# Performance work log

Measured on AMD Instinct MI355X. Metric: run time of the kernel, lower is better.

## Reference

```python
import jax, jax.numpy as jnp
import numpy as np

DIM = 768
HEADS = 12
HEAD_DIM = DIM // HEADS
HIDDEN = 4 * DIM
SCALE = HEAD_DIM ** -0.5
LN_EPS = 1e-5


def layer_norm(x, g, b):
    mu = jnp.mean(x, axis=-1, keepdims=True)
    var = jnp.var(x, axis=-1, keepdims=True)
    return (x - mu) * jax.lax.rsqrt(var + LN_EPS) * g + b


def setup_inputs() -> dict:
    key = jax.random.key(0)
    ks = jax.random.split(key, 10)
    B, N = 2, 2048
    s = 0.02
    return {
        "x": jax.random.normal(ks[0], (B, N, DIM), jnp.float32),
        "elevation": jax.random.uniform(ks[1], (B, N), jnp.float32),
        "qkv_w": jax.random.normal(ks[2], (DIM, 3 * DIM), jnp.float32) * s,
        "qkv_b": jnp.zeros((3 * DIM,), jnp.float32),
        "proj_w": jax.random.normal(ks[3], (DIM, DIM), jnp.float32) * s,
        "proj_b": jnp.zeros((DIM,), jnp.float32),
        "ln1_g": jnp.ones((DIM,), jnp.float32),
        "ln1_b": jnp.zeros((DIM,), jnp.float32),
        "ln2_g": jnp.ones((DIM,), jnp.float32),
        "ln2_b": jnp.zeros((DIM,), jnp.float32),
        "fc1_w": jax.random.normal(ks[4], (DIM, HIDDEN), jnp.float32) * s,
        "fc1_b": jnp.zeros((HIDDEN,), jnp.float32),
        "fc2_w": jax.random.normal(ks[5], (HIDDEN, DIM), jnp.float32) * s,
        "fc2_b": jnp.zeros((DIM,), jnp.float32),
        "barrier": jnp.asarray(3.0, jnp.float32),
    }


def reference(x, elevation, qkv_w, qkv_b, proj_w, proj_b, ln1_g, ln1_b,
              ln2_g, ln2_b, fc1_w, fc1_b, fc2_w, fc2_b, barrier):
    B, N, C = x.shape
    h = layer_norm(x, ln1_g, ln1_b)
    qkv = (h @ qkv_w + qkv_b).reshape(B, N, 3, HEADS, HEAD_DIM)
    q, k, v = jnp.moveaxis(qkv, 2, 0)  # each [B, N, H, D]
    # scores: [B, H, N, N]
    scores = jnp.einsum('bnhd,bmhd->bhnm', q, k) * SCALE
    w = jax.nn.softmax(scores, axis=-1)
    # pairwise elevation mask [B, N, N]: sigmoid(-s * (elev_j - elev_i))
    diff = elevation[:, None, :] - elevation[:, :, None]
    mask = jnp.clip(jax.nn.sigmoid(-barrier * diff), 1e-6, 1.0)
    w = w * mask[:, None, :, :]
    w = w / (jnp.sum(w, axis=-1, keepdims=True) + 1e-8)
    attn_out = jnp.einsum('bhnm,bmhd->bnhd', w, v).reshape(B, N, C)
    x = x + attn_out @ proj_w + proj_b
    h2 = layer_norm(x, ln2_g, ln2_b)
    mlp = jax.nn.gelu(h2 @ fc1_w + fc1_b, approximate=False) @ fc2_w + fc2_b
    return x + mlp
```

## Files before the change

kernel.cpp:

```cpp
#include <hip/hip_runtime.h>
#include <math.h>

#define DIM 768
#define HEADS 12
#define SEQ 2048
#define ROWS 4096
#define LN_EPS 1e-5f

typedef __attribute__((ext_vector_type(8))) short short8;
typedef __attribute__((ext_vector_type(4))) float floatx4;
typedef __attribute__((ext_vector_type(16))) float floatx16;
typedef unsigned short ushort_t;

__device__ __forceinline__ ushort_t f2bf(float x) {
    unsigned u = __float_as_uint(x);
    u += 0x7fff + ((u >> 16) & 1);
    return (ushort_t)(u >> 16);
}

__device__ __forceinline__ void gload_lds16(const void* g, void* l) {
    __builtin_amdgcn_global_load_lds((const __attribute__((address_space(1))) void*)g,
                                     (__attribute__((address_space(3))) void*)l, 16, 0, 0);
}

__launch_bounds__(256)
__global__ void wconv_all(const float* __restrict__ w0, const float* __restrict__ w1,
                          const float* __restrict__ w2, const float* __restrict__ w3,
                          ushort_t* __restrict__ t0, ushort_t* __restrict__ t1,
                          ushort_t* __restrict__ t2, ushort_t* __restrict__ t3) {
    __shared__ __align__(16) ushort_t s[64][72];
    int bid = blockIdx.x;
    const float* W; ushort_t* WT; int K, N, nx, id;
    if (bid < 432)       { W = w0; WT = t0; K = 768;  N = 2304; nx = 36; id = bid; }
    else if (bid < 576)  { W = w1; WT = t1; K = 768;  N = 768;  nx = 12; id = bid - 432; }
    else if (bid < 1152) { W = w2; WT = t2; K = 768;  N = 3072; nx = 48; id = bid - 576; }
    else                 { W = w3; WT = t3; K = 3072; N = 768;  nx = 12; id = bid - 1152; }
    int tx = id % nx, ty = id / nx;
    int k0 = ty * 64, n0 = tx * 64;
    int t = threadIdx.x;
    int rr0 = t >> 4, c4 = (t & 15) * 4;
    for (int rr = rr0; rr < 64; rr += 16) {
        float4 w = *(const float4*)(W + (size_t)(k0 + rr) * N + n0 + c4);
        s[c4 + 0][rr] = f2bf(w.x); s[c4 + 1][rr] = f2bf(w.y);
        s[c4 + 2][rr] = f2bf(w.z); s[c4 + 3][rr] = f2bf(w.w);
    }
    __syncthreads();
    int nl = t >> 2, kq = (t & 3) * 16;
    uint4 a = *(const uint4*)&s[nl][kq];
    uint4 b = *(const uint4*)&s[nl][kq + 8];
    *(uint4*)(WT + (size_t)(n0 + nl) * K + k0 + kq) = a;
    *(uint4*)(WT + (size_t)(n0 + nl) * K + k0 + kq + 8) = b;
}

__launch_bounds__(256)
__global__ void gelev_kernel(const float* __restrict__ elev, const float* __restrict__ barrier_p,
                             float* __restrict__ G, float* __restrict__ C2) {
    int i = blockIdx.x * 256 + threadIdx.x;
    float be = barrier_p[0] * elev[i];
    G[i]  = __expf(be);
    C2[i] = be;
}

__launch_bounds__(256)
__global__ void ln_kernel(const float* __restrict__ x, const float* __restrict__ g,
                          const float* __restrict__ b, ushort_t* __restrict__ out) {
    int row = blockIdx.x;
    const float* xr = x + (size_t)row * DIM;
    int t = threadIdx.x;
    float v0 = xr[t], v1 = xr[t + 256], v2 = xr[t + 512];
    float s  = v0 + v1 + v2;
    float ss = v0 * v0 + v1 * v1 + v2 * v2;
    #pragma unroll
    for (int o = 32; o >= 1; o >>= 1) { s += __shfl_xor(s, o); ss += __shfl_xor(ss, o); }
    __shared__ float rs[4], rss[4];
    int wid = t >> 6, lane = t & 63;
    if (lane == 0) { rs[wid] = s; rss[wid] = ss; }
    __syncthreads();
    if (t == 0) {
        float S = 0.f, SS = 0.f;
        for (int i = 0; i < 4; i++) { S += rs[i]; SS += rss[i]; }
        rs[0] = S; rss[0] = SS;
    }
    __syncthreads();
    float mean = rs[0] * (1.0f / DIM);
    float var  = rss[0] * (1.0f / DIM) - mean * mean;
    float rstd = rsqrtf(var + LN_EPS);
    ushort_t* orow = out + (size_t)row * DIM;
    orow[t]       = f2bf((v0 - mean) * rstd * g[t]       + b[t]);
    orow[t + 256] = f2bf((v1 - mean) * rstd * g[t + 256] + b[t + 256]);
    orow[t + 512] = f2bf((v2 - mean) * rstd * g[t + 512] + b[t + 512]);
}

template<int EPI>
__launch_bounds__(256)
__global__ void gemm32(const ushort_t* __restrict__ A, const ushort_t* __restrict__ WT,
                       const float* __restrict__ bias, ushort_t* __restrict__ outB,
                       ushort_t* __restrict__ qb, ushort_t* __restrict__ kb,
                       ushort_t* __restrict__ vb, int N, int K) {
    __shared__ __align__(16) ushort_t sA[128 * 32];
    __shared__ __align__(16) ushort_t sB[128 * 32];
    int t = threadIdx.x;
    int row0 = blockIdx.y * 128, col0 = blockIdx.x * 128;
    int wid = t >> 6, lane = t & 63, l31 = lane & 31, hb = lane >> 5;
    int wm = wid >> 1, wn = wid & 1;

    floatx16 acc[2][2];
    #pragma unroll
    for (int i = 0; i < 2; i++)
        #pragma unroll
        for (int j = 0; j < 2; j++)
            #pragma unroll
            for (int e = 0; e < 16; e++) acc[i][j][e] = 0.f;

    for (int k0 = 0; k0 < K; k0 += 32) {
        #pragma unroll
        for (int i = 0; i < 2; i++) {
            int c = i * 256 + t;
            int r = c >> 2, blk = c & 3;
            gload_lds16(A  + (size_t)(row0 + r) * K + k0 + ((blk ^ (r & 3)) << 3), &sA[c * 8]);
            gload_lds16(WT + (size_t)(col0 + r) * K + k0 + ((blk ^ (r & 3)) << 3), &sB[c * 8]);
        }
        __syncthreads();
        #pragma unroll
        for (int s = 0; s < 2; s++) {
            int blk = s * 2 + hb;
            int ra0 = wm * 64 + l31, ra1 = ra0 + 32;
            int rb0 = wn * 64 + l31, rb1 = rb0 + 32;
            short8 a0 = *(const short8*)&sA[ra0 * 32 + ((blk ^ (ra0 & 3)) << 3)];
            short8 a1 = *(const short8*)&sA[ra1 * 32 + ((blk ^ (ra1 & 3)) << 3)];
            short8 b0 = *(const short8*)&sB[rb0 * 32 + ((blk ^ (rb0 & 3)) << 3)];
            short8 b1 = *(const short8*)&sB[rb1 * 32 + ((blk ^ (rb1 & 3)) << 3)];
            acc[0][0] = __builtin_amdgcn_mfma_f32_32x32x16_bf16(a0, b0, acc[0][0], 0, 0, 0);
            acc[0][1] = __builtin_amdgcn_mfma_f32_32x32x16_bf16(a0, b1, acc[0][1], 0, 0, 0);
            acc[1][0] = __builtin_amdgcn_mfma_f32_32x32x16_bf16(a1, b0, acc[1][0], 0, 0, 0);
            acc[1][1] = __builtin_amdgcn_mfma_f32_32x32x16_bf16(a1, b1, acc[1][1], 0, 0, 0);
        }
        __syncthreads();
    }

    #pragma unroll
    for (int mt = 0; mt < 2; mt++) {
        #pragma unroll
        for (int nt = 0; nt < 2; nt++) {
            int gcol = col0 + wn * 64 + nt * 32 + l31;
            float bv = bias[gcol];
            if (EPI == 0) {
                int which = gcol / 768;
                int hc = gcol - which * 768;
                int hh = hc >> 6, d = hc & 63;
                #pragma unroll
                for (int rg = 0; rg < 16; rg++) {
                    int grow = row0 + wm * 64 + mt * 32 + (rg & 3) + 8 * (rg >> 2) + 4 * hb;
                    float v = acc[mt][nt][rg] + bv;
                    int b_ = grow >> 11, n = grow & 2047;
                    size_t bhh = (size_t)(b_ * 12 + hh);
                    if (which == 0)      qb[(bhh * 2048 + n) * 64 + d] = f2bf(v * 0.125f);
                    else if (which == 1) kb[(bhh * 2048 + n) * 64 + d] = f2bf(v);
                    else                 vb[(bhh * 64 + d) * 2048 + n] = f2bf(v);
                }
            } else {
                #pragma unroll
                for (int rg = 0; rg < 16; rg++) {
                    int grow = row0 + wm * 64 + mt * 32 + (rg & 3) + 8 * (rg >> 2) + 4 * hb;
                    float v = acc[mt][nt][rg] + bv;
                    v = 0.5f * v * (1.f + erff(v * 0.70710678118654752f));
                    outB[(size_t)grow * N + gcol] = f2bf(v);
                }
            }
        }
    }
}

template<int BN, int EPI>
__launch_bounds__(256)
__global__ void gemm_bf16(const ushort_t* __restrict__ A, const ushort_t* __restrict__ WT,
                          const float* __restrict__ bias, const float* __restrict__ res,
                          float* __restrict__ outF, int N, int K) {
    constexpr int NT = BN / 32;
    __shared__ __align__(16) ushort_t sA[64 * 32];
    __shared__ __align__(16) ushort_t sB[BN * 32];
    int t = threadIdx.x;
    int row0 = blockIdx.y * 64, col0 = blockIdx.x * BN;
    int wid = t >> 6, lane = t & 63;
    int wm = wid >> 1, wn = wid & 1;
    int cl = lane & 15, quad = lane >> 4;

    floatx4 acc[2][NT];
    #pragma unroll
    for (int i = 0; i < 2; i++)
        #pragma unroll
        for (int j = 0; j < NT; j++) { floatx4 z = {0.f, 0.f, 0.f, 0.f}; acc[i][j] = z; }

    for (int k0 = 0; k0 < K; k0 += 32) {
        {
            int r = t >> 2, sub = t & 3;
            gload_lds16(A + (size_t)(row0 + r) * K + k0 + sub * 8, &sA[t * 8]);
        }
        #pragma unroll
        for (int i = 0; i < BN / 64; i++) {
            int c = i * 256 + t;
            int r = c >> 2, sub = c & 3;
            gload_lds16(WT + (size_t)(col0 + r) * K + k0 + sub * 8, &sB[c * 8]);
        }
        __syncthreads();
        short8 a[2], b[NT];
        #pragma unroll
        for (int i = 0; i < 2; i++)
            a[i] = *(const short8*)&sA[(wm * 32 + i * 16 + cl) * 32 + quad * 8];
        #pragma unroll
        for (int j = 0; j < NT; j++)
            b[j] = *(const short8*)&sB[(wn * (BN / 2) + j * 16 + cl) * 32 + quad * 8];
        #pragma unroll
        for (int i = 0; i < 2; i++)
            #pragma unroll
            for (int j = 0; j < NT; j++)
                acc[i][j] = __builtin_amdgcn_mfma_f32_16x16x32_bf16(a[i], b[j], acc[i][j], 0, 0, 0);
        __syncthreads();
    }

    #pragma unroll
    for (int i = 0; i < 2; i++) {
        #pragma unroll
        for (int j = 0; j < NT; j++) {
            int gcol = col0 + wn * (BN / 2) + j * 16 + cl;
            float bv = bias[gcol];
            #pragma unroll
            for (int rg = 0; rg < 4; rg++) {
                int grow = row0 + wm * 32 + i * 16 + quad * 4 + rg;
                float v = acc[i][j][rg] + bv + res[(size_t)grow * N + gcol];
                outF[(size_t)grow * N + gcol] = v;
            }
        }
    }
}

__launch_bounds__(256)
__global__ void attn_mfma(const ushort_t* __restrict__ qb, const ushort_t* __restrict__ kb,
                          const ushort_t* __restrict__ vb, const float* __restrict__ G,
                          const float* __restrict__ C2, ushort_t* __restrict__ attn) {
    __shared__ __align__(16) ushort_t Qs[4096];
    __shared__ __align__(16) ushort_t Ks[2][4096];
    __shared__ __align__(16) ushort_t Vt[2][4096];
    __shared__ __align__(16) ushort_t Ps[4096];
    __shared__ float semL[2][64];
    int qt = blockIdx.x, hh = blockIdx.y, b = blockIdx.z;
    int t = threadIdx.x, wid = t >> 6, lane = t & 63, l31 = lane & 31, hb = lane >> 5;
    int wm = wid >> 1, wn = wid & 1;
    int q0 = qt * 64;
    size_t bh = (size_t)(b * 12 + hh);

    const ushort_t* qbase = qb + (bh * 2048 + q0) * 64;
    #pragma unroll
    for (int i = 0; i < 2; i++) {
        int c = i * 256 + t, row = c >> 3, blk = c & 7;
        gload_lds16(qbase + (row << 6) + ((blk ^ (row & 7)) << 3), &Qs[c * 8]);
    }

    float gi[16]; floatx16 c2v;
    #pragma unroll
    for (int rg = 0; rg < 16; rg++) {
        int rr = (rg & 3) + 8 * (rg >> 2) + 4 * hb;
        int gr = b * 2048 + q0 + wm * 32 + rr;
        gi[rg] = G[gr]; c2v[rg] = C2[gr];
    }

    {
        const ushort_t* kbase = kb + bh * 2048 * 64;
        const ushort_t* vbase = vb + bh * 131072;
        #pragma unroll
        for (int i = 0; i < 2; i++) {
            int c = i * 256 + t, row = c >> 3, blk = c & 7;
            gload_lds16(kbase + (row << 6) + ((blk ^ (row & 7)) << 3), &Ks[0][c * 8]);
            gload_lds16(vbase + (size_t)row * 2048 + ((blk ^ (row & 7)) << 3), &Vt[0][c * 8]);
        }
    }

    floatx16 o0, o1;
    float semP[16];
    #pragma unroll
    for (int e = 0; e < 16; e++) { o0[e] = 0.f; o1[e] = 0.f; semP[e] = 0.f; }

    int arow = wm * 32 + l31, brow = wn * 32 + l31, x7 = l31 & 7;

    for (int kt = 0; kt < 32; kt++) {
        int cur = kt & 1;
        __syncthreads();
        if (kt < 31) {
            int k0n = (kt + 1) * 64;
            const ushort_t* kbase = kb + (bh * 2048 + k0n) * 64;
            const ushort_t* vbase = vb + bh * 131072 + k0n;
            #pragma unroll
            for (int i = 0; i < 2; i++) {
                int c = i * 256 + t, row = c >> 3, blk = c & 7;
                gload_lds16(kbase + (row << 6) + ((blk ^ (row & 7)) << 3), &Ks[cur ^ 1][c * 8]);
                gload_lds16(vbase + (size_t)row * 2048 + ((blk ^ (row & 7)) << 3), &Vt[cur ^ 1][c * 8]);
            }
        }
        float gj = G[b * 2048 + kt * 64 + wn * 32 + l31];

        floatx16 s = c2v;
        #pragma unroll
        for (int s4 = 0; s4 < 4; s4++) {
            short8 aq = *(const short8*)&Qs[(arow << 6) + (((s4 * 2 + hb) ^ x7) << 3)];
            short8 bk = *(const short8*)&Ks[cur][(brow << 6) + (((s4 * 2 + hb) ^ x7) << 3)];
            s = __builtin_amdgcn_mfma_f32_32x32x16_bf16(aq, bk, s, 0, 0, 0);
        }

        #pragma unroll
        for (int rg = 0; rg < 16; rg++) {
            int rr = (rg & 3) + 8 * (rg >> 2) + 4 * hb;
            int qrow = wm * 32 + rr;
            float tf = __expf(s[rg]);
            float p  = tf * __builtin_amdgcn_rcpf(gi[rg] + gj);
            semP[rg] += p;
            Ps[(qrow << 6) + (((wn * 4 + (l31 >> 3)) ^ (qrow & 7)) << 3) + (l31 & 7)] =
                (ushort_t)(__float_as_uint(p) >> 16);
        }

        #pragma unroll
        for (int s2 = 0; s2 < 2; s2++) {
            int blk = wn * 4 + s2 * 2 + hb;
            short8 ap  = *(const short8*)&Ps[(arow << 6) + ((blk ^ x7) << 3)];
            short8 bv0 = *(const short8*)&Vt[cur][(l31 << 6) + ((blk ^ x7) << 3)];
            short8 bv1 = *(const short8*)&Vt[cur][((32 + l31) << 6) + ((blk ^ x7) << 3)];
            o0 = __builtin_amdgcn_mfma_f32_32x32x16_bf16(ap, bv0, o0, 0, 0, 0);
            o1 = __builtin_amdgcn_mfma_f32_32x32x16_bf16(ap, bv1, o1, 0, 0, 0);
        }
    }

    #pragma unroll
    for (int rg = 0; rg < 16; rg++) {
        float v = semP[rg];
        v += __shfl_xor(v, 1);  v += __shfl_xor(v, 2);  v += __shfl_xor(v, 4);
        v += __shfl_xor(v, 8);  v += __shfl_xor(v, 16);
        semP[rg] = v;
    }
    #pragma unroll
    for (int rg = 0; rg < 16; rg++) {
        int rr = (rg & 3) + 8 * (rg >> 2) + 4 * hb;
        if (l31 == rr) semL[wn][wm * 32 + rr] = semP[rg];
    }
    __syncthreads();
    float* oL = (float*)Ks;
    if (wn == 0) {
        #pragma unroll
        for (int rg = 0; rg < 16; rg++) {
            int rr = (rg & 3) + 8 * (rg >> 2) + 4 * hb;
            oL[wm * 2048 + (rr << 6) + l31]      = o0[rg];
            oL[wm * 2048 + (rr << 6) + 32 + l31] = o1[rg];
        }
    }
    __syncthreads();
    if (wn == 1) {
        #pragma unroll
        for (int rg = 0; rg < 16; rg++) {
            int rr = (rg & 3) + 8 * (rg >> 2) + 4 * hb;
            int qrow = wm * 32 + rr;
            float inv = __builtin_amdgcn_rcpf(semL[0][qrow] + semL[1][qrow]);
            float v0 = o0[rg] + oL[wm * 2048 + (rr << 6) + l31];
            float v1 = o1[rg] + oL[wm * 2048 + (rr << 6) + 32 + l31];
            Ps[(qrow << 6) + ((((l31 >> 3)) ^ (qrow & 7)) << 3) + (l31 & 7)]     = f2bf(v0 * inv);
            Ps[(qrow << 6) + (((4 + (l31 >> 3)) ^ (qrow & 7)) << 3) + (l31 & 7)] = f2bf(v1 * inv);
        }
    }
    __syncthreads();
    int row = t >> 2, ch = t & 3;
    uint4 u0 = *(const uint4*)&Ps[(row << 6) + (((ch * 2    ) ^ (row & 7)) << 3)];
    uint4 u1 = *(const uint4*)&Ps[(row << 6) + (((ch * 2 + 1) ^ (row & 7)) << 3)];
    size_t oa = (size_t)(b * 2048 + q0 + row) * 768 + hh * 64 + ch * 16;
    *(uint4*)(attn + oa)     = u0;
    *(uint4*)(attn + oa + 8) = u1;
}

extern "C" void kernel_launch(void* const* d_in, const int* in_sizes, int n_in,
                              void* d_out, int out_size, void* d_ws, size_t ws_size,
                              hipStream_t stream) {
    const float* x      = (const float*)d_in[0];
    const float* elev   = (const float*)d_in[1];
    const float* qkv_w  = (const float*)d_in[2];
    const float* qkv_b  = (const float*)d_in[3];
    const float* proj_w = (const float*)d_in[4];
    const float* proj_b = (const float*)d_in[5];
    const float* ln1_g  = (const float*)d_in[6];
    const float* ln1_b  = (const float*)d_in[7];
    const float* ln2_g  = (const float*)d_in[8];
    const float* ln2_b  = (const float*)d_in[9];
    const float* fc1_w  = (const float*)d_in[10];
    const float* fc1_b  = (const float*)d_in[11];
    const float* fc2_w  = (const float*)d_in[12];
    const float* fc2_b  = (const float*)d_in[13];
    const float* barrier= (const float*)d_in[14];
    float* out = (float*)d_out;
    char* ws = (char*)d_ws;

    ushort_t* h    = (ushort_t*)(ws + 0);
    ushort_t* qb   = (ushort_t*)(ws + 6291456);
    ushort_t* kb   = (ushort_t*)(ws + 12582912);
    ushort_t* vb   = (ushort_t*)(ws + 18874368);
    ushort_t* f1   = (ushort_t*)(ws + 0);
    ushort_t* attn = (ushort_t*)(ws + 25165824);
    ushort_t* h2   = (ushort_t*)(ws + 31457280);
    float*    Gf   = (float*)(ws + 31457280);
    float*    C2f  = (float*)(ws + 31473664);
    ushort_t* qkvT = (ushort_t*)(ws + 37748736);
    ushort_t* projT= (ushort_t*)(ws + 41287680);
    ushort_t* fc1T = (ushort_t*)(ws + 42467328);
    ushort_t* fc2T = (ushort_t*)(ws + 47185920);

    wconv_all<<<1728, 256, 0, stream>>>(qkv_w, proj_w, fc1_w, fc2_w, qkvT, projT, fc1T, fc2T);
    gelev_kernel<<<16, 256, 0, stream>>>(elev, barrier, Gf, C2f);

    ln_kernel<<<ROWS, 256, 0, stream>>>(x, ln1_g, ln1_b, h);
    gemm32<0><<<dim3(2304 / 128, 32), 256, 0, stream>>>(
        h, qkvT, qkv_b, nullptr, qb, kb, vb, 2304, 768);
    attn_mfma<<<dim3(32, HEADS, 2), 256, 0, stream>>>(qb, kb, vb, Gf, C2f, attn);
    gemm_bf16<64, 2><<<dim3(768 / 64, 64), 256, 0, stream>>>(
        attn, projT, proj_b, x, out, 768, 768);
    ln_kernel<<<ROWS, 256, 0, stream>>>(out, ln2_g, ln2_b, h2);
    gemm32<1><<<dim3(3072 / 128, 32), 256, 0, stream>>>(
        h2, fc1T, fc1_b, f1, nullptr, nullptr, nullptr, 3072, 768);
    gemm_bf16<64, 2><<<dim3(768 / 64, 64), 256, 0, stream>>>(
        f1, fc2T, fc2_b, out, out, 768, 3072);
}
```

Measured before the change: 346.6 us.

## Restructure attention kernel to 16x16 MFMA with per-wave row ownership

The attention kernel now gives each of the four waves 16 query rows across the full 64-key tile and uses 16x16x32 bf16 MFMAs, replacing the 2x2 wave split over 32x32 tiles. This removes the cross-wave reduction of partial outputs and row sums through shared memory, along with its extra barriers, at the end of the kernel. The K/V double buffer is split into named buffers and the loop is unrolled by two so buffer selection is static. Results are written straight to global memory as scattered 2-byte stores instead of staged 16-byte vector stores, and each wave now issues more, smaller MFMAs per tile.

```diff
diff --git a/kernel.cpp b/kernel.cpp
--- a/kernel.cpp
+++ b/kernel.cpp
@@ -234,20 +234,77 @@
     }
 }
 
+
+#define PREFETCH(K0N, KSN, VTN)                                                   \
+    {                                                                             \
+        const ushort_t* kbase_ = kb + (bh * 2048 + (K0N)) * 64;                   \
+        const ushort_t* vbase_ = vb + bh * 131072 + (K0N);                        \
+        int c0_ = t, r0_ = c0_ >> 3, b0_ = c0_ & 7;                               \
+        gload_lds16(kbase_ + (r0_ << 6) + ((b0_ ^ (r0_ & 7)) << 3), &KSN[c0_ * 8]); \
+        gload_lds16(vbase_ + (size_t)r0_ * 2048 + ((b0_ ^ (r0_ & 7)) << 3), &VTN[c0_ * 8]); \
+        int c1_ = 256 + t, r1_ = c1_ >> 3, b1_ = c1_ & 7;                         \
+        gload_lds16(kbase_ + (r1_ << 6) + ((b1_ ^ (r1_ & 7)) << 3), &KSN[c1_ * 8]); \
+        gload_lds16(vbase_ + (size_t)r1_ * 2048 + ((b1_ ^ (r1_ & 7)) << 3), &VTN[c1_ * 8]); \
+    }
+
+#define ATTN_TILE(KT, KSC, VTC, KSN, VTN)                                         \
+    {                                                                             \
+        __syncthreads();                                                          \
+        if ((KT) < 31) PREFETCH(((KT) + 1) * 64, KSN, VTN)                        \
+        float gjv_[4];                                                            \
+        gjv_[0] = G[b * 2048 + (KT) * 64 + cl];                                   \
+        gjv_[1] = G[b * 2048 + (KT) * 64 + 16 + cl];                              \
+        gjv_[2] = G[b * 2048 + (KT) * 64 + 32 + cl];                              \
+        gjv_[3] = G[b * 2048 + (KT) * 64 + 48 + cl];                              \
+        floatx4 s_[4];                                                            \
+        s_[0] = c2init; s_[1] = c2init; s_[2] = c2init; s_[3] = c2init;           \
+        _Pragma("unroll")                                                         \
+        for (int kh = 0; kh < 2; kh++) {                                          \
+            short8 aq_ = *(const short8*)&Qs[((wid * 16 + cl) << 6) + (((kh * 4 + quad) ^ (cl & 7)) << 3)]; \
+            _Pragma("unroll")                                                     \
+            for (int nt = 0; nt < 4; nt++) {                                      \
+                short8 bk_ = *(const short8*)&KSC[((nt * 16 + cl) << 6) + (((kh * 4 + quad) ^ (cl & 7)) << 3)]; \
+                s_[nt] = __builtin_amdgcn_mfma_f32_16x16x32_bf16(aq_, bk_, s_[nt], 0, 0, 0); \
+            }                                                                     \
+        }                                                                         \
+        _Pragma("unroll")                                                         \
+        for (int rg = 0; rg < 4; rg++) {                                          \
+            int prow_ = wid * 16 + quad * 4 + rg;                                 \
+            int r8_ = prow_ & 7, pb_ = prow_ << 6, cs_ = cl & 7, ch_ = cl >> 3;   \
+            _Pragma("unroll")                                                     \
+            for (int nt = 0; nt < 4; nt++) {                                      \
+                float tf_ = __expf(s_[nt][rg]);                                   \
+                float p_  = tf_ * __builtin_amdgcn_rcpf(gi[rg] + gjv_[nt]);       \
+                sem[rg] += p_;                                                    \
+                Ps[pb_ + (((nt * 2 + ch_) ^ r8_) << 3) + cs_] = (ushort_t)(__float_as_uint(p_) >> 16); \
+            }                                                                     \
+        }                                                                         \
+        _Pragma("unroll")                                                         \
+        for (int kh = 0; kh < 2; kh++) {                                          \
+            short8 ap_ = *(const short8*)&Ps[((wid * 16 + cl) << 6) + (((kh * 4 + quad) ^ (cl & 7)) << 3)]; \
+            _Pragma("unroll")                                                     \
+            for (int dt = 0; dt < 4; dt++) {                                      \
+                short8 bv_ = *(const short8*)&VTC[((dt * 16 + cl) << 6) + (((kh * 4 + quad) ^ (cl & 7)) << 3)]; \
+                o[dt] = __builtin_amdgcn_mfma_f32_16x16x32_bf16(ap_, bv_, o[dt], 0, 0, 0); \
+            }                                                                     \
+        }                                                                         \
+    }
+
 __launch_bounds__(256)
 __global__ void attn_mfma(const ushort_t* __restrict__ qb, const ushort_t* __restrict__ kb,
                           const ushort_t* __restrict__ vb, const float* __restrict__ G,
                           const float* __restrict__ C2, ushort_t* __restrict__ attn) {
     __shared__ __align__(16) ushort_t Qs[4096];
-    __shared__ __align__(16) ushort_t Ks[2][4096];
-    __shared__ __align__(16) ushort_t Vt[2][4096];
+    __shared__ __align__(16) ushort_t Ks0[4096];
+    __shared__ __align__(16) ushort_t Ks1[4096];
+    __shared__ __align__(16) ushort_t Vt0[4096];
+    __shared__ __align__(16) ushort_t Vt1[4096];
     __shared__ __align__(16) ushort_t Ps[4096];
-    __shared__ float semL[2][64];
-    int qt = blockIdx.x, hh = blockIdx.y, b = blockIdx.z;
-    int t = threadIdx.x, wid = t >> 6, lane = t & 63, l31 = lane & 31, hb = lane >> 5;
-    int wm = wid >> 1, wn = wid & 1;
+    int qt = blockIdx.x, h = blockIdx.y, b = blockIdx.z;
+    int t = threadIdx.x, wid = t >> 6, lane = t & 63;
+    int cl = lane & 15, quad = lane >> 4;
     int q0 = qt * 64;
-    size_t bh = (size_t)(b * 12 + hh);
+    size_t bh = (size_t)(b * 12 + h);
 
     const ushort_t* qbase = qb + (bh * 2048 + q0) * 64;
     #pragma unroll
@@ -255,121 +312,35 @@
         int c = i * 256 + t, row = c >> 3, blk = c & 7;
         gload_lds16(qbase + (row << 6) + ((blk ^ (row & 7)) << 3), &Qs[c * 8]);
     }
-
-    float gi[16]; floatx16 c2v;
-    #pragma unroll
-    for (int rg = 0; rg < 16; rg++) {
-        int rr = (rg & 3) + 8 * (rg >> 2) + 4 * hb;
-        int gr = b * 2048 + q0 + wm * 32 + rr;
-        gi[rg] = G[gr]; c2v[rg] = C2[gr];
-    }
-
-    {
-        const ushort_t* kbase = kb + bh * 2048 * 64;
-        const ushort_t* vbase = vb + bh * 131072;
-        #pragma unroll
-        for (int i = 0; i < 2; i++) {
-            int c = i * 256 + t, row = c >> 3, blk = c & 7;
-            gload_lds16(kbase + (row << 6) + ((blk ^ (row & 7)) << 3), &Ks[0][c * 8]);
-            gload_lds16(vbase + (size_t)row * 2048 + ((blk ^ (row & 7)) << 3), &Vt[0][c * 8]);
-        }
-    }
-
-    floatx16 o0, o1;
-    float semP[16];
-    #pragma unroll
-    for (int e = 0; e < 16; e++) { o0[e] = 0.f; o1[e] = 0.f; semP[e] = 0.f; }
-
-    int arow = wm * 32 + l31, brow = wn * 32 + l31, x7 = l31 & 7;
-
-    for (int kt = 0; kt < 32; kt++) {
-        int cur = kt & 1;
-        __syncthreads();
-        if (kt < 31) {
-            int k0n = (kt + 1) * 64;
-            const ushort_t* kbase = kb + (bh * 2048 + k0n) * 64;
-            const ushort_t* vbase = vb + bh * 131072 + k0n;
-            #pragma unroll
-            for (int i = 0; i < 2; i++) {
-                int c = i * 256 + t, row = c >> 3, blk = c & 7;
-                gload_lds16(kbase + (row << 6) + ((blk ^ (row & 7)) << 3), &Ks[cur ^ 1][c * 8]);
-                gload_lds16(vbase + (size_t)row * 2048 + ((blk ^ (row & 7)) << 3), &Vt[cur ^ 1][c * 8]);
-            }
-        }
-        float gj = G[b * 2048 + kt * 64 + wn * 32 + l31];
-
-        floatx16 s = c2v;
-        #pragma unroll
-        for (int s4 = 0; s4 < 4; s4++) {
-            short8 aq = *(const short8*)&Qs[(arow << 6) + (((s4 * 2 + hb) ^ x7) << 3)];
-            short8 bk = *(const short8*)&Ks[cur][(brow << 6) + (((s4 * 2 + hb) ^ x7) << 3)];
-            s = __builtin_amdgcn_mfma_f32_32x32x16_bf16(aq, bk, s, 0, 0, 0);
-        }
-
-        #pragma unroll
-        for (int rg = 0; rg < 16; rg++) {
-            int rr = (rg & 3) + 8 * (rg >> 2) + 4 * hb;
-            int qrow = wm * 32 + rr;
-            float tf = __expf(s[rg]);
-            float p  = tf * __builtin_amdgcn_rcpf(gi[rg] + gj);
-            semP[rg] += p;
-            Ps[(qrow << 6) + (((wn * 4 + (l31 >> 3)) ^ (qrow & 7)) << 3) + (l31 & 7)] =
-                (ushort_t)(__float_as_uint(p) >> 16);
-        }
-
-        #pragma unroll
-        for (int s2 = 0; s2 < 2; s2++) {
-            int blk = wn * 4 + s2 * 2 + hb;
-            short8 ap  = *(const short8*)&Ps[(arow << 6) + ((blk ^ x7) << 3)];
-            short8 bv0 = *(const short8*)&Vt[cur][(l31 << 6) + ((blk ^ x7) << 3)];
-            short8 bv1 = *(const short8*)&Vt[cur][((32 + l31) << 6) + ((blk ^ x7) << 3)];
-            o0 = __builtin_amdgcn_mfma_f32_32x32x16_bf16(ap, bv0, o0, 0, 0, 0);
-            o1 = __builtin_amdgcn_mfma_f32_32x32x16_bf16(ap, bv1, o1, 0, 0, 0);
-        }
-    }
-
-    #pragma unroll
-    for (int rg = 0; rg < 16; rg++) {
-        float v = semP[rg];
-        v += __shfl_xor(v, 1);  v += __shfl_xor(v, 2);  v += __shfl_xor(v, 4);
-        v += __shfl_xor(v, 8);  v += __shfl_xor(v, 16);
-        semP[rg] = v;
-    }
-    #pragma unroll
-    for (int rg = 0; rg < 16; rg++) {
-        int rr = (rg & 3) + 8 * (rg >> 2) + 4 * hb;
-        if (l31 == rr) semL[wn][wm * 32 + rr] = semP[rg];
-    }
-    __syncthreads();
-    float* oL = (float*)Ks;
-    if (wn == 0) {
-        #pragma unroll
-        for (int rg = 0; rg < 16; rg++) {
-            int rr = (rg & 3) + 8 * (rg >> 2) + 4 * hb;
-            oL[wm * 2048 + (rr << 6) + l31]      = o0[rg];
-            oL[wm * 2048 + (rr << 6) + 32 + l31] = o1[rg];
-        }
-    }
-    __syncthreads();
-    if (wn == 1) {
-        #pragma unroll
-        for (int rg = 0; rg < 16; rg++) {
-            int rr = (rg & 3) + 8 * (rg >> 2) + 4 * hb;
-            int qrow = wm * 32 + rr;
-            float inv = __builtin_amdgcn_rcpf(semL[0][qrow] + semL[1][qrow]);
-            float v0 = o0[rg] + oL[wm * 2048 + (rr << 6) + l31];
-            float v1 = o1[rg] + oL[wm * 2048 + (rr << 6) + 32 + l31];
-            Ps[(qrow << 6) + ((((l31 >> 3)) ^ (qrow & 7)) << 3) + (l31 & 7)]     = f2bf(v0 * inv);
-            Ps[(qrow << 6) + (((4 + (l31 >> 3)) ^ (qrow & 7)) << 3) + (l31 & 7)] = f2bf(v1 * inv);
-        }
-    }
-    __syncthreads();
-    int row = t >> 2, ch = t & 3;
-    uint4 u0 = *(const uint4*)&Ps[(row << 6) + (((ch * 2    ) ^ (row & 7)) << 3)];
-    uint4 u1 = *(const uint4*)&Ps[(row << 6) + (((ch * 2 + 1) ^ (row & 7)) << 3)];
-    size_t oa = (size_t)(b * 2048 + q0 + row) * 768 + hh * 64 + ch * 16;
-    *(uint4*)(attn + oa)     = u0;
-    *(uint4*)(attn + oa + 8) = u1;
+    int qrow4 = b * 2048 + q0 + wid * 16 + quad * 4;
+    float4 g4  = *(const float4*)(G  + qrow4);
+    float4 c24 = *(const float4*)(C2 + qrow4);
+    float gi[4]  = {g4.x, g4.y, g4.z, g4.w};
+    floatx4 c2init = {c24.x, c24.y, c24.z, c24.w};
+
+    PREFETCH(0, Ks0, Vt0)
+
+    floatx4 o[4];
+    #pragma unroll
+    for (int j = 0; j < 4; j++) { floatx4 z = {0.f, 0.f, 0.f, 0.f}; o[j] = z; }
+    float sem[4] = {0.f, 0.f, 0.f, 0.f};
+
+    for (int kt = 0; kt < 32; kt += 2) {
+        ATTN_TILE(kt,     Ks0, Vt0, Ks1, Vt1)
+        ATTN_TILE(kt + 1, Ks1, Vt1, Ks0, Vt0)
+    }
+
+    #pragma unroll
+    for (int rg = 0; rg < 4; rg++) {
+        float m = sem[rg];
+        #pragma unroll
+        for (int off = 1; off < 16; off <<= 1) m += __shfl_xor(m, off);
+        float inv = __builtin_amdgcn_rcpf(m);
+        int grow = b * 2048 + q0 + wid * 16 + quad * 4 + rg;
+        #pragma unroll
+        for (int dt = 0; dt < 4; dt++)
+            attn[(size_t)grow * 768 + h * 64 + dt * 16 + cl] = f2bf(o[dt][rg] * inv);
+    }
 }
 
 extern "C" void kernel_launch(void* const* d_in, const int* in_sizes, int n_in,
```

New measurement: 324.4 us. 6.4% less time.
